# Kernel optimization log

Measured on AMD Instinct MI355X. Metric: run time of the kernel, lower is better.

The kernel has to match this reference:

```python
import jax, jax.numpy as jnp
import numpy as np

NL = 256
NP = 8192
NV = 16
B = 2


def _xavier(key, shape):
    fan_in, fan_out = shape[-2], shape[-1]
    lim = np.sqrt(6.0 / (fan_in + fan_out))
    return jax.random.uniform(key, shape, jnp.float32, -lim, lim)


def setup_inputs() -> dict:
    key = jax.random.key(0)
    ks = jax.random.split(key, 12)
    return {
        "nodes": jax.random.normal(ks[0], (B, NP, NL), jnp.float32),
        "edges_attributes": jax.random.normal(ks[1], (NP, NV, NL), jnp.float32),
        "edges_indices": jax.random.randint(ks[2], (NP, NV), 0, NP, jnp.int64) if jax.config.jax_enable_x64 else jax.random.randint(ks[2], (NP, NV), 0, NP).astype(jnp.int32),
        # edge MLP (dim_in=3*NL, nb_hidden=3 -> first + 2 hidden + last)
        "e_fw": _xavier(ks[3], (3 * NL, NL)), "e_fb": jnp.zeros((NL,), jnp.float32),
        "e_hw": _xavier(ks[4], (2, NL, NL)), "e_hb": jnp.zeros((2, NL), jnp.float32),
        "e_lw": _xavier(ks[5], (NL, NL)), "e_lb": jnp.zeros((NL,), jnp.float32),
        # node MLP (dim_in=2*NL)
        "n_fw": _xavier(ks[6], (2 * NL, NL)), "n_fb": jnp.zeros((NL,), jnp.float32),
        "n_hw": _xavier(ks[7], (2, NL, NL)), "n_hb": jnp.zeros((2, NL), jnp.float32),
        "n_lw": _xavier(ks[8], (NL, NL)), "n_lb": jnp.zeros((NL,), jnp.float32),
    }


def _mlp(x, fw, fb, hw, hb, lw, lb):
    x = jax.nn.relu(x @ fw + fb)
    for i in range(hw.shape[0]):  # fixed small number of hidden layers
        x = jax.nn.relu(x @ hw[i] + hb[i])
    return x @ lw + lb


def reference(nodes, edges_attributes, edges_indices,
              e_fw, e_fb, e_hw, e_hb, e_lw, e_lb,
              n_fw, n_fb, n_hw, n_hb, n_lw, n_lb):
    b, npts, nl = nodes.shape
    nv = edges_indices.shape[1]
    # gather neighbor features: [B, Np, Nv, Nl]
    nodes_nb = jnp.take(nodes, edges_indices, axis=1)
    # self features broadcast over neighbor axis, edge attrs broadcast over batch
    self_exp = jnp.broadcast_to(nodes[:, :, None, :], (b, npts, nv, nl))
    edge_exp = jnp.broadcast_to(edges_attributes[None], (b, npts, nv, nl))
    concat_msg = jnp.concatenate([self_exp, nodes_nb, edge_exp], axis=-1)  # [B,Np,Nv,3Nl]
    new_edges = _mlp(concat_msg, e_fw, e_fb, e_hw, e_hb, e_lw, e_lb)  # [B,Np,Nv,Nl]
    agg = jnp.sum(new_edges, axis=2)  # [B,Np,Nl]
    concat_nodes = jnp.concatenate([nodes, agg], axis=-1)  # [B,Np,2Nl]
    new_nodes = nodes + _mlp(concat_nodes, n_fw, n_fb, n_hw, n_hb, n_lw, n_lb)
    return new_nodes, new_edges[0]
```

## Files before the change

### kernel.cpp

```cpp
#include <hip/hip_runtime.h>
#include <hip/hip_bf16.h>


typedef __bf16 bf16;
typedef __bf16 bf16x8 __attribute__((ext_vector_type(8)));
typedef float f32x4 __attribute__((ext_vector_type(4)));

#define MFMA16(a, b, c) __builtin_amdgcn_mfma_f32_16x16x32_bf16((a), (b), (c), 0, 0, 0)

constexpr int kNP = 8192;
constexpr int kNV = 16;

__global__ __launch_bounds__(256) void pack_all(
    const float* __restrict__ e_fw, const float* __restrict__ e_hw,
    const float* __restrict__ e_lw, const float* __restrict__ n_fw,
    const float* __restrict__ n_hw, const float* __restrict__ n_lw,
    bf16* __restrict__ wp) {
  int t = blockIdx.x * 256 + threadIdx.x;
  const float* src;
  int kd = 8, local;
  if (t < 196608) {
    src = e_fw + (t >> 16) * 65536; local = t & 65535;
  } else if (t < 262144) { src = e_hw;           local = t - 196608;
  } else if (t < 327680) { src = e_hw + 65536;   local = t - 262144;
  } else if (t < 393216) { src = e_lw;           local = t - 327680;
  } else if (t < 524288) { src = n_fw;           local = t - 393216; kd = 16;
  } else if (t < 589824) { src = n_hw;           local = t - 524288;
  } else if (t < 655360) { src = n_hw + 65536;   local = t - 589824;
  } else               { src = n_lw;             local = t - 655360; }
  int j = local & 7;
  int l = (local >> 3) & 63;
  int r2 = local >> 9;
  int ks = r2 % kd;
  int nt = r2 / kd;
  int k = ks * 32 + ((l >> 4) << 3) + j;
  int n = (nt << 4) + (l & 15);
  wp[t] = (bf16)src[k * 256 + n];
}

template <int KD, int MT>
__device__ __forceinline__ void layer_acc(const bf16* X, int xs,
                                          const bf16* __restrict__ Wp,
                                          const float* __restrict__ bias,
                                          f32x4 (&acc)[MT][4], int rowOff,
                                          int wc) {
  const int lane = threadIdx.x & 63;
  const int q = lane >> 4;
  const int c = lane & 15;
#pragma unroll
  for (int nt = 0; nt < 4; nt++) {
    float bv = bias ? bias[wc * 64 + nt * 16 + c] : 0.0f;
#pragma unroll
    for (int mt = 0; mt < MT; mt++) {
      acc[mt][nt][0] = bv; acc[mt][nt][1] = bv;
      acc[mt][nt][2] = bv; acc[mt][nt][3] = bv;
    }
  }
#pragma unroll
  for (int ks = 0; ks < KD; ks++) {
    bf16x8 a[MT];
#pragma unroll
    for (int mt = 0; mt < MT; mt++)
      a[mt] = *(const bf16x8*)(X + (rowOff + mt * 16 + c) * xs + ks * 32 + q * 8);
    bf16x8 bb[4];
#pragma unroll
    for (int nt = 0; nt < 4; nt++)
      bb[nt] = *(const bf16x8*)(Wp + ((((wc * 4 + nt) * KD + ks) * 64 + lane) << 3));
#pragma unroll
    for (int mt = 0; mt < MT; mt++)
#pragma unroll
      for (int nt = 0; nt < 4; nt++)
        acc[mt][nt] = MFMA16(a[mt], bb[nt], acc[mt][nt]);
  }
}

template <int KD, int MT, bool RELU>
__device__ __forceinline__ void layer_inplace(bf16* X, int xs_r, int xs_w,
                                              const bf16* __restrict__ Wp,
                                              const float* __restrict__ bias,
                                              int rowOff, int wc) {
  f32x4 acc[MT][4];
  layer_acc<KD, MT>(X, xs_r, Wp, bias, acc, rowOff, wc);
  const int lane = threadIdx.x & 63;
  const int q = lane >> 4;
  const int c = lane & 15;
  __syncthreads();
#pragma unroll
  for (int mt = 0; mt < MT; mt++)
#pragma unroll
    for (int nt = 0; nt < 4; nt++)
#pragma unroll
      for (int i = 0; i < 4; i++) {
        float v = acc[mt][nt][i];
        if (RELU) v = fmaxf(v, 0.0f);
        X[(rowOff + mt * 16 + q * 4 + i) * xs_w + (wc * 64 + nt * 16 + c)] = (bf16)v;
      }
  __syncthreads();
}

__global__ __launch_bounds__(512, 4) void producer_sp(
    const float* __restrict__ nodes, const bf16* __restrict__ w_self,
    const bf16* __restrict__ w_nb, const float* __restrict__ e_fb,
    bf16* __restrict__ Sb, bf16* __restrict__ Pb) {
  __shared__ bf16 X[64 * 280];
  const int t = threadIdx.x;
  const int m0 = blockIdx.x * 64;
  {
    const int r = t >> 3;
    const int q8 = t & 7;
#pragma unroll
    for (int c8 = 0; c8 < 4; c8++) {
      int col = q8 * 8 + c8 * 64;
      float4 f0 = *(const float4*)(nodes + (m0 + r) * 256 + col);
      float4 f1 = *(const float4*)(nodes + (m0 + r) * 256 + col + 4);
      bf16x8 v;
      v[0] = (bf16)f0.x; v[1] = (bf16)f0.y; v[2] = (bf16)f0.z; v[3] = (bf16)f0.w;
      v[4] = (bf16)f1.x; v[5] = (bf16)f1.y; v[6] = (bf16)f1.z; v[7] = (bf16)f1.w;
      *(bf16x8*)(X + r * 280 + col) = v;
    }
  }
  __syncthreads();
  const int lane = t & 63;
  const int w = t >> 6;
  const int wc = w & 3;
  const int rowOff = (w >> 2) * 32;
  const int q = lane >> 4;
  const int c = lane & 15;
  f32x4 acc[2][4];
  layer_acc<8, 2>(X, 280, w_self, e_fb, acc, rowOff, wc);
#pragma unroll
  for (int mt = 0; mt < 2; mt++)
#pragma unroll
    for (int nt = 0; nt < 4; nt++)
#pragma unroll
      for (int i = 0; i < 4; i++)
        Sb[(m0 + rowOff + mt * 16 + q * 4 + i) * 256 + wc * 64 + nt * 16 + c] =
            (bf16)acc[mt][nt][i];
  layer_acc<8, 2>(X, 280, w_nb, nullptr, acc, rowOff, wc);
#pragma unroll
  for (int mt = 0; mt < 2; mt++)
#pragma unroll
    for (int nt = 0; nt < 4; nt++)
#pragma unroll
      for (int i = 0; i < 4; i++)
        Pb[(m0 + rowOff + mt * 16 + q * 4 + i) * 256 + wc * 64 + nt * 16 + c] =
            (bf16)acc[mt][nt][i];
}

__global__ __launch_bounds__(512, 4) void edge_mlp(
    const bf16* __restrict__ S, const bf16* __restrict__ P,
    const float* __restrict__ eattr, const int* __restrict__ idx,
    const bf16* __restrict__ w_ea, const bf16* __restrict__ Wh0,
    const bf16* __restrict__ Wh1, const bf16* __restrict__ Wl,
    const float* __restrict__ e_hb, const float* __restrict__ e_lb,
    bf16* __restrict__ agg, float* __restrict__ out_edges) {
  __shared__ bf16 X[64 * 280];
  const int t = threadIdx.x;
  const int pbase = blockIdx.x * 2;
  {
    const int r = t >> 4;
    const int q16 = t & 15;
    const float* src = eattr + (pbase * 16 + r) * 256 + q16 * 16;
    bf16* dst = X + (32 + r) * 280 + q16 * 16;
    float4 f0 = *(const float4*)(src);
    float4 f1 = *(const float4*)(src + 4);
    float4 f2 = *(const float4*)(src + 8);
    float4 f3 = *(const float4*)(src + 12);
    bf16x8 v0, v1;
    v0[0] = (bf16)f0.x; v0[1] = (bf16)f0.y; v0[2] = (bf16)f0.z; v0[3] = (bf16)f0.w;
    v0[4] = (bf16)f1.x; v0[5] = (bf16)f1.y; v0[6] = (bf16)f1.z; v0[7] = (bf16)f1.w;
    v1[0] = (bf16)f2.x; v1[1] = (bf16)f2.y; v1[2] = (bf16)f2.z; v1[3] = (bf16)f2.w;
    v1[4] = (bf16)f3.x; v1[5] = (bf16)f3.y; v1[6] = (bf16)f3.z; v1[7] = (bf16)f3.w;
    *(bf16x8*)(dst) = v0;
    *(bf16x8*)(dst + 8) = v1;
  }
  __syncthreads();
  const int lane = t & 63;
  const int w = t >> 6;
  const int wc = w & 3;
  const int rg = w >> 2;
  const int q = lane >> 4;
  const int c = lane & 15;
  {
    f32x4 acce[1][4];
    layer_acc<8, 1>(X, 280, w_ea, nullptr, acce, 32 + rg * 16, wc);
    __syncthreads();
#pragma unroll
    for (int nt = 0; nt < 4; nt++)
#pragma unroll
      for (int i = 0; i < 4; i++)
        X[(32 + rg * 16 + q * 4 + i) * 280 + wc * 64 + nt * 16 + c] =
            (bf16)acce[0][nt][i];
  }
  __syncthreads();
  {
    const int r = t >> 3;
    const int q8 = t & 7;
    const int b = r >> 5;
    const int rr = r & 31;
    const int p = pbase + (rr >> 4);
    const int v = rr & 15;
    const int nb = idx[p * kNV + v];
    const bf16* Srow = S + ((b << 13) + p) * 256;
    const bf16* Prow = P + ((b << 13) + nb) * 256;
    bf16x8 hold[4];
#pragma unroll
    for (int j = 0; j < 4; j++) {
      int col = q8 * 32 + j * 8;
      bf16x8 ev = *(const bf16x8*)(X + (32 + rr) * 280 + col);
      bf16x8 sv = *(const bf16x8*)(Srow + col);
      bf16x8 pv = *(const bf16x8*)(Prow + col);
      bf16x8 o;
#pragma unroll
      for (int k = 0; k < 8; k++) {
        float f = (float)sv[k] + (float)pv[k] + (float)ev[k];
        o[k] = (bf16)fmaxf(f, 0.0f);
      }
      hold[j] = o;
    }
    __syncthreads();
#pragma unroll
    for (int j = 0; j < 4; j++)
      *(bf16x8*)(X + r * 280 + q8 * 32 + j * 8) = hold[j];
  }
  __syncthreads();
  layer_inplace<8, 2, true>(X, 280, 280, Wh0, e_hb, rg * 32, wc);
  layer_inplace<8, 2, true>(X, 280, 280, Wh1, e_hb + 256, rg * 32, wc);
  f32x4 acc[2][4];
  layer_acc<8, 2>(X, 280, Wl, e_lb, acc, rg * 32, wc);
#pragma unroll
  for (int mt = 0; mt < 2; mt++) {
    const int g = rg * 2 + mt;
#pragma unroll
    for (int nt = 0; nt < 4; nt++) {
      float s = acc[mt][nt][0] + acc[mt][nt][1] + acc[mt][nt][2] + acc[mt][nt][3];
      s += __shfl_xor(s, 16, 64);
      s += __shfl_xor(s, 32, 64);
      if (lane < 16)
        agg[(((g >> 1) << 13) + pbase + (g & 1)) * 256 + wc * 64 + nt * 16 + lane] =
            (bf16)s;
    }
  }
  if (rg == 0) {
#pragma unroll
    for (int mt = 0; mt < 2; mt++)
#pragma unroll
      for (int nt = 0; nt < 4; nt++)
#pragma unroll
        for (int i = 0; i < 4; i++) {
          int e = (pbase + mt) * kNV + q * 4 + i;
          out_edges[e * 256 + wc * 64 + nt * 16 + c] = acc[mt][nt][i];
        }
  }
}

__global__ __launch_bounds__(512, 4) void node_mlp(
    const float* __restrict__ nodes, const bf16* __restrict__ agg,
    const bf16* __restrict__ Wf, const bf16* __restrict__ Wh0,
    const bf16* __restrict__ Wh1, const bf16* __restrict__ Wl,
    const float* __restrict__ n_fb, const float* __restrict__ n_hb,
    const float* __restrict__ n_lb, float* __restrict__ out_nodes) {
  __shared__ bf16 X[32 * 536];
  const int t = threadIdx.x;
  const int r = t >> 4;
  const int q16 = t & 15;
  const int m = blockIdx.x * 32 + r;
#pragma unroll
  for (int c8 = 0; c8 < 4; c8++) {
    int col = q16 * 8 + c8 * 128;
    if (col < 256) {
      float4 f0 = *(const float4*)(nodes + m * 256 + col);
      float4 f1 = *(const float4*)(nodes + m * 256 + col + 4);
      bf16x8 v;
      v[0] = (bf16)f0.x; v[1] = (bf16)f0.y; v[2] = (bf16)f0.z; v[3] = (bf16)f0.w;
      v[4] = (bf16)f1.x; v[5] = (bf16)f1.y; v[6] = (bf16)f1.z; v[7] = (bf16)f1.w;
      *(bf16x8*)(X + r * 536 + col) = v;
    } else {
      *(bf16x8*)(X + r * 536 + col) =
          *(const bf16x8*)(agg + m * 256 + (col - 256));
    }
  }
  __syncthreads();
  const int w = t >> 6;
  const int wc = w & 3;
  const int rowOff = (w >> 2) * 16;
  layer_inplace<16, 1, true>(X, 536, 280, Wf, n_fb, rowOff, wc);
  layer_inplace<8, 1, true>(X, 280, 280, Wh0, n_hb, rowOff, wc);
  layer_inplace<8, 1, true>(X, 280, 280, Wh1, n_hb + 256, rowOff, wc);
  f32x4 acc[1][4];
  layer_acc<8, 1>(X, 280, Wl, n_lb, acc, rowOff, wc);
  const int lane = t & 63;
  const int q = lane >> 4;
  const int c = lane & 15;
#pragma unroll
  for (int nt = 0; nt < 4; nt++)
#pragma unroll
    for (int i = 0; i < 4; i++) {
      int mm = blockIdx.x * 32 + rowOff + q * 4 + i;
      int col = wc * 64 + nt * 16 + c;
      out_nodes[mm * 256 + col] = nodes[mm * 256 + col] + acc[0][nt][i];
    }
}

extern "C" void kernel_launch(void* const* d_in, const int* in_sizes, int n_in,
                              void* d_out, int out_size, void* d_ws,
                              size_t ws_size, hipStream_t stream) {
  const float* nodes = (const float*)d_in[0];
  const float* eattr = (const float*)d_in[1];
  const int* eidx = (const int*)d_in[2];
  const float* e_fw = (const float*)d_in[3];
  const float* e_fb = (const float*)d_in[4];
  const float* e_hw = (const float*)d_in[5];
  const float* e_hb = (const float*)d_in[6];
  const float* e_lw = (const float*)d_in[7];
  const float* e_lb = (const float*)d_in[8];
  const float* n_fw = (const float*)d_in[9];
  const float* n_fb = (const float*)d_in[10];
  const float* n_hw = (const float*)d_in[11];
  const float* n_hb = (const float*)d_in[12];
  const float* n_lw = (const float*)d_in[13];
  const float* n_lb = (const float*)d_in[14];

  char* ws = (char*)d_ws;
  bf16* Sb = (bf16*)(ws + 0);
  bf16* Pb = (bf16*)(ws + 8388608);
  bf16* aggb = (bf16*)(ws + 16777216);
  bf16* wp = (bf16*)(ws + 25165824);
  bf16* w_self = wp;
  bf16* w_nb = wp + 65536;
  bf16* w_ea = wp + 131072;
  bf16* w_eh0 = wp + 196608;
  bf16* w_eh1 = wp + 262144;
  bf16* w_el = wp + 327680;
  bf16* w_nf = wp + 393216;
  bf16* w_nh0 = wp + 524288;
  bf16* w_nh1 = wp + 589824;
  bf16* w_nl = wp + 655360;

  float* out_nodes = (float*)d_out;
  float* out_edges = (float*)d_out + 4194304;

  pack_all<<<2816, 256, 0, stream>>>(e_fw, e_hw, e_lw, n_fw, n_hw, n_lw, wp);
  producer_sp<<<256, 512, 0, stream>>>(nodes, w_self, w_nb, e_fb, Sb, Pb);
  edge_mlp<<<4096, 512, 0, stream>>>(Sb, Pb, eattr, eidx, w_ea, w_eh0, w_eh1,
                                     w_el, e_hb, e_lb, aggb, out_edges);
  node_mlp<<<512, 512, 0, stream>>>(nodes, aggb, w_nf, w_nh0, w_nh1, w_nl,
                                    n_fb, n_hb, n_lb, out_nodes);
}
```

Baseline: 470.9 us.

## Halve block sizes across kernels and vectorize weight packing per MFMA tile

```diff
diff --git a/kernel.cpp b/kernel.cpp
--- a/kernel.cpp
+++ b/kernel.cpp
@@ -16,26 +16,32 @@
     const float* __restrict__ e_lw, const float* __restrict__ n_fw,
     const float* __restrict__ n_hw, const float* __restrict__ n_lw,
     bf16* __restrict__ wp) {
-  int t = blockIdx.x * 256 + threadIdx.x;
+  const int s = blockIdx.x;
   const float* src;
-  int kd = 8, local;
-  if (t < 196608) {
-    src = e_fw + (t >> 16) * 65536; local = t & 65535;
-  } else if (t < 262144) { src = e_hw;           local = t - 196608;
-  } else if (t < 327680) { src = e_hw + 65536;   local = t - 262144;
-  } else if (t < 393216) { src = e_lw;           local = t - 327680;
-  } else if (t < 524288) { src = n_fw;           local = t - 393216; kd = 16;
-  } else if (t < 589824) { src = n_hw;           local = t - 524288;
-  } else if (t < 655360) { src = n_hw + 65536;   local = t - 589824;
-  } else               { src = n_lw;             local = t - 655360; }
-  int j = local & 7;
-  int l = (local >> 3) & 63;
-  int r2 = local >> 9;
-  int ks = r2 % kd;
-  int nt = r2 / kd;
-  int k = ks * 32 + ((l >> 4) << 3) + j;
-  int n = (nt << 4) + (l & 15);
-  wp[t] = (bf16)src[k * 256 + n];
+  bf16* dst;
+  int ks, kd = 8;
+  if (s < 24)      { src = e_fw + (s >> 3) * 65536; dst = wp + (s >> 3) * 65536; ks = s & 7; }
+  else if (s < 32) { src = e_hw;          dst = wp + 196608; ks = s - 24; }
+  else if (s < 40) { src = e_hw + 65536;  dst = wp + 262144; ks = s - 32; }
+  else if (s < 48) { src = e_lw;          dst = wp + 327680; ks = s - 40; }
+  else if (s < 64) { src = n_fw;          dst = wp + 393216; ks = s - 48; kd = 16; }
+  else if (s < 72) { src = n_hw;          dst = wp + 524288; ks = s - 64; }
+  else if (s < 80) { src = n_hw + 65536;  dst = wp + 589824; ks = s - 72; }
+  else             { src = n_lw;          dst = wp + 655360; ks = s - 80; }
+  const int t = threadIdx.x;
+  const int lane = t & 63;
+  const int w = t >> 6;
+  const int q = lane >> 4;
+  const int c = lane & 15;
+#pragma unroll
+  for (int nti = 0; nti < 4; nti++) {
+    const int nt = w * 4 + nti;
+    bf16x8 v;
+#pragma unroll
+    for (int j = 0; j < 8; j++)
+      v[j] = (bf16)src[(ks * 32 + q * 8 + j) * 256 + nt * 16 + c];
+    *(bf16x8*)(dst + (((nt * kd + ks) * 64 + lane) << 3)) = v;
+  }
 }
 
 template <int KD, int MT>
@@ -98,70 +104,18 @@
   __syncthreads();
 }
 
-__global__ __launch_bounds__(512, 4) void producer_sp(
+__global__ __launch_bounds__(256, 8) void producer_sp(
     const float* __restrict__ nodes, const bf16* __restrict__ w_self,
     const bf16* __restrict__ w_nb, const float* __restrict__ e_fb,
     bf16* __restrict__ Sb, bf16* __restrict__ Pb) {
-  __shared__ bf16 X[64 * 280];
+  __shared__ bf16 X[16 * 280];
   const int t = threadIdx.x;
-  const int m0 = blockIdx.x * 64;
-  {
-    const int r = t >> 3;
-    const int q8 = t & 7;
-#pragma unroll
-    for (int c8 = 0; c8 < 4; c8++) {
-      int col = q8 * 8 + c8 * 64;
-      float4 f0 = *(const float4*)(nodes + (m0 + r) * 256 + col);
-      float4 f1 = *(const float4*)(nodes + (m0 + r) * 256 + col + 4);
-      bf16x8 v;
-      v[0] = (bf16)f0.x; v[1] = (bf16)f0.y; v[2] = (bf16)f0.z; v[3] = (bf16)f0.w;
-      v[4] = (bf16)f1.x; v[5] = (bf16)f1.y; v[6] = (bf16)f1.z; v[7] = (bf16)f1.w;
-      *(bf16x8*)(X + r * 280 + col) = v;
-    }
-  }
-  __syncthreads();
-  const int lane = t & 63;
-  const int w = t >> 6;
-  const int wc = w & 3;
-  const int rowOff = (w >> 2) * 32;
-  const int q = lane >> 4;
-  const int c = lane & 15;
-  f32x4 acc[2][4];
-  layer_acc<8, 2>(X, 280, w_self, e_fb, acc, rowOff, wc);
-#pragma unroll
-  for (int mt = 0; mt < 2; mt++)
-#pragma unroll
-    for (int nt = 0; nt < 4; nt++)
-#pragma unroll
-      for (int i = 0; i < 4; i++)
-        Sb[(m0 + rowOff + mt * 16 + q * 4 + i) * 256 + wc * 64 + nt * 16 + c] =
-            (bf16)acc[mt][nt][i];
-  layer_acc<8, 2>(X, 280, w_nb, nullptr, acc, rowOff, wc);
-#pragma unroll
-  for (int mt = 0; mt < 2; mt++)
-#pragma unroll
-    for (int nt = 0; nt < 4; nt++)
-#pragma unroll
-      for (int i = 0; i < 4; i++)
-        Pb[(m0 + rowOff + mt * 16 + q * 4 + i) * 256 + wc * 64 + nt * 16 + c] =
-            (bf16)acc[mt][nt][i];
-}
-
-__global__ __launch_bounds__(512, 4) void edge_mlp(
-    const bf16* __restrict__ S, const bf16* __restrict__ P,
-    const float* __restrict__ eattr, const int* __restrict__ idx,
-    const bf16* __restrict__ w_ea, const bf16* __restrict__ Wh0,
-    const bf16* __restrict__ Wh1, const bf16* __restrict__ Wl,
-    const float* __restrict__ e_hb, const float* __restrict__ e_lb,
-    bf16* __restrict__ agg, float* __restrict__ out_edges) {
-  __shared__ bf16 X[64 * 280];
-  const int t = threadIdx.x;
-  const int pbase = blockIdx.x * 2;
+  const int m0 = blockIdx.x * 16;
   {
     const int r = t >> 4;
     const int q16 = t & 15;
-    const float* src = eattr + (pbase * 16 + r) * 256 + q16 * 16;
-    bf16* dst = X + (32 + r) * 280 + q16 * 16;
+    const float* src = nodes + (m0 + r) * 256 + q16 * 16;
+    bf16* dst = X + r * 280 + q16 * 16;
     float4 f0 = *(const float4*)(src);
     float4 f1 = *(const float4*)(src + 4);
     float4 f2 = *(const float4*)(src + 8);
@@ -176,30 +130,72 @@
   }
   __syncthreads();
   const int lane = t & 63;
-  const int w = t >> 6;
-  const int wc = w & 3;
-  const int rg = w >> 2;
+  const int wc = t >> 6;
+  const int q = lane >> 4;
+  const int c = lane & 15;
+  f32x4 acc[1][4];
+  layer_acc<8, 1>(X, 280, w_self, e_fb, acc, 0, wc);
+#pragma unroll
+  for (int nt = 0; nt < 4; nt++)
+#pragma unroll
+    for (int i = 0; i < 4; i++)
+      Sb[(m0 + q * 4 + i) * 256 + wc * 64 + nt * 16 + c] = (bf16)acc[0][nt][i];
+  layer_acc<8, 1>(X, 280, w_nb, nullptr, acc, 0, wc);
+#pragma unroll
+  for (int nt = 0; nt < 4; nt++)
+#pragma unroll
+    for (int i = 0; i < 4; i++)
+      Pb[(m0 + q * 4 + i) * 256 + wc * 64 + nt * 16 + c] = (bf16)acc[0][nt][i];
+}
+
+__global__ __launch_bounds__(256, 6) void edge_mlp(
+    const bf16* __restrict__ S, const bf16* __restrict__ P,
+    const float* __restrict__ eattr, const int* __restrict__ idx,
+    const bf16* __restrict__ w_ea, const bf16* __restrict__ Wh0,
+    const bf16* __restrict__ Wh1, const bf16* __restrict__ Wl,
+    const float* __restrict__ e_hb, const float* __restrict__ e_lb,
+    bf16* __restrict__ agg, float* __restrict__ out_edges) {
+  __shared__ bf16 X[32 * 280];
+  const int t = threadIdx.x;
+  const int p = blockIdx.x;
+  {
+    const int r = t >> 4;
+    const int q16 = t & 15;
+    const float* src = eattr + (p * 16 + r) * 256 + q16 * 16;
+    bf16* dst = X + (16 + r) * 280 + q16 * 16;
+    float4 f0 = *(const float4*)(src);
+    float4 f1 = *(const float4*)(src + 4);
+    float4 f2 = *(const float4*)(src + 8);
+    float4 f3 = *(const float4*)(src + 12);
+    bf16x8 v0, v1;
+    v0[0] = (bf16)f0.x; v0[1] = (bf16)f0.y; v0[2] = (bf16)f0.z; v0[3] = (bf16)f0.w;
+    v0[4] = (bf16)f1.x; v0[5] = (bf16)f1.y; v0[6] = (bf16)f1.z; v0[7] = (bf16)f1.w;
+    v1[0] = (bf16)f2.x; v1[1] = (bf16)f2.y; v1[2] = (bf16)f2.z; v1[3] = (bf16)f2.w;
+    v1[4] = (bf16)f3.x; v1[5] = (bf16)f3.y; v1[6] = (bf16)f3.z; v1[7] = (bf16)f3.w;
+    *(bf16x8*)(dst) = v0;
+    *(bf16x8*)(dst + 8) = v1;
+  }
+  __syncthreads();
+  const int lane = t & 63;
+  const int wc = t >> 6;
   const int q = lane >> 4;
   const int c = lane & 15;
   {
     f32x4 acce[1][4];
-    layer_acc<8, 1>(X, 280, w_ea, nullptr, acce, 32 + rg * 16, wc);
+    layer_acc<8, 1>(X, 280, w_ea, nullptr, acce, 16, wc);
     __syncthreads();
 #pragma unroll
     for (int nt = 0; nt < 4; nt++)
 #pragma unroll
       for (int i = 0; i < 4; i++)
-        X[(32 + rg * 16 + q * 4 + i) * 280 + wc * 64 + nt * 16 + c] =
-            (bf16)acce[0][nt][i];
+        X[(16 + q * 4 + i) * 280 + wc * 64 + nt * 16 + c] = (bf16)acce[0][nt][i];
   }
   __syncthreads();
   {
     const int r = t >> 3;
     const int q8 = t & 7;
-    const int b = r >> 5;
-    const int rr = r & 31;
-    const int p = pbase + (rr >> 4);
-    const int v = rr & 15;
+    const int b = r >> 4;
+    const int v = r & 15;
     const int nb = idx[p * kNV + v];
     const bf16* Srow = S + ((b << 13) + p) * 256;
     const bf16* Prow = P + ((b << 13) + nb) * 256;
@@ -207,7 +203,7 @@
 #pragma unroll
     for (int j = 0; j < 4; j++) {
       int col = q8 * 32 + j * 8;
-      bf16x8 ev = *(const bf16x8*)(X + (32 + rr) * 280 + col);
+      bf16x8 ev = *(const bf16x8*)(X + (16 + v) * 280 + col);
       bf16x8 sv = *(const bf16x8*)(Srow + col);
       bf16x8 pv = *(const bf16x8*)(Prow + col);
       bf16x8 o;
@@ -224,71 +220,67 @@
       *(bf16x8*)(X + r * 280 + q8 * 32 + j * 8) = hold[j];
   }
   __syncthreads();
-  layer_inplace<8, 2, true>(X, 280, 280, Wh0, e_hb, rg * 32, wc);
-  layer_inplace<8, 2, true>(X, 280, 280, Wh1, e_hb + 256, rg * 32, wc);
+  layer_inplace<8, 2, true>(X, 280, 280, Wh0, e_hb, 0, wc);
+  layer_inplace<8, 2, true>(X, 280, 280, Wh1, e_hb + 256, 0, wc);
   f32x4 acc[2][4];
-  layer_acc<8, 2>(X, 280, Wl, e_lb, acc, rg * 32, wc);
+  layer_acc<8, 2>(X, 280, Wl, e_lb, acc, 0, wc);
 #pragma unroll
   for (int mt = 0; mt < 2; mt++) {
-    const int g = rg * 2 + mt;
 #pragma unroll
     for (int nt = 0; nt < 4; nt++) {
       float s = acc[mt][nt][0] + acc[mt][nt][1] + acc[mt][nt][2] + acc[mt][nt][3];
       s += __shfl_xor(s, 16, 64);
       s += __shfl_xor(s, 32, 64);
       if (lane < 16)
-        agg[(((g >> 1) << 13) + pbase + (g & 1)) * 256 + wc * 64 + nt * 16 + lane] =
-            (bf16)s;
-    }
-  }
-  if (rg == 0) {
-#pragma unroll
-    for (int mt = 0; mt < 2; mt++)
-#pragma unroll
-      for (int nt = 0; nt < 4; nt++)
-#pragma unroll
-        for (int i = 0; i < 4; i++) {
-          int e = (pbase + mt) * kNV + q * 4 + i;
-          out_edges[e * 256 + wc * 64 + nt * 16 + c] = acc[mt][nt][i];
-        }
-  }
-}
-
-__global__ __launch_bounds__(512, 4) void node_mlp(
+        agg[((mt << 13) + p) * 256 + wc * 64 + nt * 16 + lane] = (bf16)s;
+    }
+  }
+#pragma unroll
+  for (int nt = 0; nt < 4; nt++)
+#pragma unroll
+    for (int i = 0; i < 4; i++) {
+      int e = p * kNV + q * 4 + i;
+      out_edges[e * 256 + wc * 64 + nt * 16 + c] = acc[0][nt][i];
+    }
+}
+
+__global__ __launch_bounds__(256, 8) void node_mlp(
     const float* __restrict__ nodes, const bf16* __restrict__ agg,
     const bf16* __restrict__ Wf, const bf16* __restrict__ Wh0,
     const bf16* __restrict__ Wh1, const bf16* __restrict__ Wl,
     const float* __restrict__ n_fb, const float* __restrict__ n_hb,
     const float* __restrict__ n_lb, float* __restrict__ out_nodes) {
-  __shared__ bf16 X[32 * 536];
+  __shared__ bf16 X[16 * 536];
   const int t = threadIdx.x;
   const int r = t >> 4;
   const int q16 = t & 15;
-  const int m = blockIdx.x * 32 + r;
-#pragma unroll
-  for (int c8 = 0; c8 < 4; c8++) {
-    int col = q16 * 8 + c8 * 128;
-    if (col < 256) {
-      float4 f0 = *(const float4*)(nodes + m * 256 + col);
-      float4 f1 = *(const float4*)(nodes + m * 256 + col + 4);
+  const int m = blockIdx.x * 16 + r;
+  if (q16 < 8) {
+    const float* src = nodes + m * 256 + q16 * 32;
+    bf16* dst = X + r * 536 + q16 * 32;
+#pragma unroll
+    for (int h = 0; h < 4; h++) {
+      float4 f0 = *(const float4*)(src + h * 8);
+      float4 f1 = *(const float4*)(src + h * 8 + 4);
       bf16x8 v;
       v[0] = (bf16)f0.x; v[1] = (bf16)f0.y; v[2] = (bf16)f0.z; v[3] = (bf16)f0.w;
       v[4] = (bf16)f1.x; v[5] = (bf16)f1.y; v[6] = (bf16)f1.z; v[7] = (bf16)f1.w;
-      *(bf16x8*)(X + r * 536 + col) = v;
-    } else {
-      *(bf16x8*)(X + r * 536 + col) =
-          *(const bf16x8*)(agg + m * 256 + (col - 256));
-    }
-  }
-  __syncthreads();
-  const int w = t >> 6;
-  const int wc = w & 3;
-  const int rowOff = (w >> 2) * 16;
-  layer_inplace<16, 1, true>(X, 536, 280, Wf, n_fb, rowOff, wc);
-  layer_inplace<8, 1, true>(X, 280, 280, Wh0, n_hb, rowOff, wc);
-  layer_inplace<8, 1, true>(X, 280, 280, Wh1, n_hb + 256, rowOff, wc);
+      *(bf16x8*)(dst + h * 8) = v;
+    }
+  } else {
+    const bf16* src = agg + m * 256 + (q16 - 8) * 32;
+    bf16* dst = X + r * 536 + 256 + (q16 - 8) * 32;
+#pragma unroll
+    for (int h = 0; h < 4; h++)
+      *(bf16x8*)(dst + h * 8) = *(const bf16x8*)(src + h * 8);
+  }
+  __syncthreads();
+  const int wc = t >> 6;
+  layer_inplace<16, 1, true>(X, 536, 280, Wf, n_fb, 0, wc);
+  layer_inplace<8, 1, true>(X, 280, 280, Wh0, n_hb, 0, wc);
+  layer_inplace<8, 1, true>(X, 280, 280, Wh1, n_hb + 256, 0, wc);
   f32x4 acc[1][4];
-  layer_acc<8, 1>(X, 280, Wl, n_lb, acc, rowOff, wc);
+  layer_acc<8, 1>(X, 280, Wl, n_lb, acc, 0, wc);
   const int lane = t & 63;
   const int q = lane >> 4;
   const int c = lane & 15;
@@ -296,7 +288,7 @@
   for (int nt = 0; nt < 4; nt++)
 #pragma unroll
     for (int i = 0; i < 4; i++) {
-      int mm = blockIdx.x * 32 + rowOff + q * 4 + i;
+      int mm = blockIdx.x * 16 + q * 4 + i;
       int col = wc * 64 + nt * 16 + c;
       out_nodes[mm * 256 + col] = nodes[mm * 256 + col] + acc[0][nt][i];
     }
@@ -340,10 +332,10 @@
   float* out_nodes = (float*)d_out;
   float* out_edges = (float*)d_out + 4194304;
 
-  pack_all<<<2816, 256, 0, stream>>>(e_fw, e_hw, e_lw, n_fw, n_hw, n_lw, wp);
-  producer_sp<<<256, 512, 0, stream>>>(nodes, w_self, w_nb, e_fb, Sb, Pb);
-  edge_mlp<<<4096, 512, 0, stream>>>(Sb, Pb, eattr, eidx, w_ea, w_eh0, w_eh1,
+  pack_all<<<88, 256, 0, stream>>>(e_fw, e_hw, e_lw, n_fw, n_hw, n_lw, wp);
+  producer_sp<<<1024, 256, 0, stream>>>(nodes, w_self, w_nb, e_fb, Sb, Pb);
+  edge_mlp<<<8192, 256, 0, stream>>>(Sb, Pb, eattr, eidx, w_ea, w_eh0, w_eh1,
                                      w_el, e_hb, e_lb, aggb, out_edges);
-  node_mlp<<<512, 512, 0, stream>>>(nodes, aggb, w_nf, w_nh0, w_nh1, w_nl,
-                                    n_fb, n_hb, n_lb, out_nodes);
-}
+  node_mlp<<<1024, 256, 0, stream>>>(nodes, aggb, w_nf, w_nh0, w_nh1, w_nl,
+                                     n_fb, n_hb, n_lb, out_nodes);
+}
```

Result: slower. 556.4 us (+18.1%).

## Use 32x32x16 MFMA for edge MLP hidden and last layers with repacked weights

Applied to the files above, without the earlier changes.

```diff
diff --git a/kernel.cpp b/kernel.cpp
--- a/kernel.cpp
+++ b/kernel.cpp
@@ -5,8 +5,10 @@
 typedef __bf16 bf16;
 typedef __bf16 bf16x8 __attribute__((ext_vector_type(8)));
 typedef float f32x4 __attribute__((ext_vector_type(4)));
+typedef float f32x16 __attribute__((ext_vector_type(16)));
 
 #define MFMA16(a, b, c) __builtin_amdgcn_mfma_f32_16x16x32_bf16((a), (b), (c), 0, 0, 0)
+#define MFMA32(a, b, c) __builtin_amdgcn_mfma_f32_32x32x16_bf16((a), (b), (c), 0, 0, 0)
 
 constexpr int kNP = 8192;
 constexpr int kNV = 16;
@@ -16,26 +18,49 @@
     const float* __restrict__ e_lw, const float* __restrict__ n_fw,
     const float* __restrict__ n_hw, const float* __restrict__ n_lw,
     bf16* __restrict__ wp) {
-  int t = blockIdx.x * 256 + threadIdx.x;
-  const float* src;
-  int kd = 8, local;
-  if (t < 196608) {
-    src = e_fw + (t >> 16) * 65536; local = t & 65535;
-  } else if (t < 262144) { src = e_hw;           local = t - 196608;
-  } else if (t < 327680) { src = e_hw + 65536;   local = t - 262144;
-  } else if (t < 393216) { src = e_lw;           local = t - 327680;
-  } else if (t < 524288) { src = n_fw;           local = t - 393216; kd = 16;
-  } else if (t < 589824) { src = n_hw;           local = t - 524288;
-  } else if (t < 655360) { src = n_hw + 65536;   local = t - 589824;
-  } else               { src = n_lw;             local = t - 655360; }
-  int j = local & 7;
-  int l = (local >> 3) & 63;
-  int r2 = local >> 9;
-  int ks = r2 % kd;
-  int nt = r2 / kd;
-  int k = ks * 32 + ((l >> 4) << 3) + j;
-  int n = (nt << 4) + (l & 15);
-  wp[t] = (bf16)src[k * 256 + n];
+  const int s = blockIdx.x;
+  const int t = threadIdx.x;
+  const int lane = t & 63;
+  const int w = t >> 6;
+  if (s < 64) {
+    const float* src;
+    bf16* dst;
+    int ks, kd = 8;
+    if (s < 24)      { src = e_fw + (s >> 3) * 65536; dst = wp + (s >> 3) * 65536; ks = s & 7; }
+    else if (s < 40) { src = n_fw;          dst = wp + 393216; ks = s - 24; kd = 16; }
+    else if (s < 48) { src = n_hw;          dst = wp + 524288; ks = s - 40; }
+    else if (s < 56) { src = n_hw + 65536;  dst = wp + 589824; ks = s - 48; }
+    else             { src = n_lw;          dst = wp + 655360; ks = s - 56; }
+    const int q = lane >> 4;
+    const int c = lane & 15;
+#pragma unroll
+    for (int nti = 0; nti < 4; nti++) {
+      const int nt = w * 4 + nti;
+      bf16x8 v;
+#pragma unroll
+      for (int j = 0; j < 8; j++)
+        v[j] = (bf16)src[(ks * 32 + q * 8 + j) * 256 + nt * 16 + c];
+      *(bf16x8*)(dst + (((nt * kd + ks) * 64 + lane) << 3)) = v;
+    }
+  } else {
+    const int s2 = s - 64;
+    const int mat = s2 >> 4;
+    const int ks = s2 & 15;
+    const float* src = (mat == 0) ? e_hw : (mat == 1) ? (e_hw + 65536) : e_lw;
+    bf16* dst = wp + 196608 + mat * 65536;
+    const int ko = lane >> 5;
+    const int col = lane & 31;
+#pragma unroll
+    for (int h = 0; h < 2; h++) {
+      const int wcnt = w * 2 + h;
+      bf16x8 v;
+#pragma unroll
+      for (int j = 0; j < 8; j++)
+        v[j] = (bf16)src[(ks * 16 + ko * 8 + j) * 256 + wcnt * 32 + col];
+      *(bf16x8*)(dst + (((wcnt * 16 + ks) * 64 + lane) << 3));
+      *(bf16x8*)(dst + (((wcnt * 16 + ks) * 64 + lane) << 3)) = v;
+    }
+  }
 }
 
 template <int KD, int MT>
@@ -95,6 +120,56 @@
         if (RELU) v = fmaxf(v, 0.0f);
         X[(rowOff + mt * 16 + q * 4 + i) * xs_w + (wc * 64 + nt * 16 + c)] = (bf16)v;
       }
+  __syncthreads();
+}
+
+template <int KD2>
+__device__ __forceinline__ void layer_acc32(const bf16* X, int xs,
+                                            const bf16* __restrict__ Wp,
+                                            const float* __restrict__ bias,
+                                            f32x16 (&acc)[2], int rowOff,
+                                            int wc) {
+  const int lane = threadIdx.x & 63;
+  const int row = lane & 31;
+  const int ko = lane >> 5;
+  const int col = lane & 31;
+#pragma unroll
+  for (int nt = 0; nt < 2; nt++) {
+    float bv = bias ? bias[wc * 64 + nt * 32 + col] : 0.0f;
+#pragma unroll
+    for (int r = 0; r < 16; r++) acc[nt][r] = bv;
+  }
+#pragma unroll
+  for (int ks = 0; ks < KD2; ks++) {
+    bf16x8 a = *(const bf16x8*)(X + (rowOff + row) * xs + ks * 16 + ko * 8);
+#pragma unroll
+    for (int nt = 0; nt < 2; nt++) {
+      bf16x8 b = *(const bf16x8*)(Wp + ((((wc * 2 + nt) * KD2 + ks) * 64 + lane) << 3));
+      acc[nt] = MFMA32(a, b, acc[nt]);
+    }
+  }
+}
+
+template <int KD2, bool RELU>
+__device__ __forceinline__ void layer_inplace32(bf16* X, int xs,
+                                                const bf16* __restrict__ Wp,
+                                                const float* __restrict__ bias,
+                                                int rowOff, int wc) {
+  f32x16 acc[2];
+  layer_acc32<KD2>(X, xs, Wp, bias, acc, rowOff, wc);
+  const int lane = threadIdx.x & 63;
+  const int h = lane >> 5;
+  const int col = lane & 31;
+  __syncthreads();
+#pragma unroll
+  for (int nt = 0; nt < 2; nt++)
+#pragma unroll
+    for (int r = 0; r < 16; r++) {
+      float v = acc[nt][r];
+      if (RELU) v = fmaxf(v, 0.0f);
+      const int rr = (r & 3) + 8 * (r >> 2) + 4 * h;
+      X[(rowOff + rr) * xs + (wc * 64 + nt * 32 + col)] = (bf16)v;
+    }
   __syncthreads();
 }
 
@@ -224,33 +299,32 @@
       *(bf16x8*)(X + r * 280 + q8 * 32 + j * 8) = hold[j];
   }
   __syncthreads();
-  layer_inplace<8, 2, true>(X, 280, 280, Wh0, e_hb, rg * 32, wc);
-  layer_inplace<8, 2, true>(X, 280, 280, Wh1, e_hb + 256, rg * 32, wc);
-  f32x4 acc[2][4];
-  layer_acc<8, 2>(X, 280, Wl, e_lb, acc, rg * 32, wc);
-#pragma unroll
-  for (int mt = 0; mt < 2; mt++) {
-    const int g = rg * 2 + mt;
-#pragma unroll
-    for (int nt = 0; nt < 4; nt++) {
-      float s = acc[mt][nt][0] + acc[mt][nt][1] + acc[mt][nt][2] + acc[mt][nt][3];
-      s += __shfl_xor(s, 16, 64);
+  layer_inplace32<16, true>(X, 280, Wh0, e_hb, rg * 32, wc);
+  layer_inplace32<16, true>(X, 280, Wh1, e_hb + 256, rg * 32, wc);
+  f32x16 acc[2];
+  layer_acc32<16>(X, 280, Wl, e_lb, acc, rg * 32, wc);
+  const int col = lane & 31;
+#pragma unroll
+  for (int nt = 0; nt < 2; nt++) {
+#pragma unroll
+    for (int pp = 0; pp < 2; pp++) {
+      float s = 0.0f;
+#pragma unroll
+      for (int r8 = 0; r8 < 8; r8++) s += acc[nt][pp * 8 + r8];
       s += __shfl_xor(s, 32, 64);
-      if (lane < 16)
-        agg[(((g >> 1) << 13) + pbase + (g & 1)) * 256 + wc * 64 + nt * 16 + lane] =
-            (bf16)s;
+      if (lane < 32)
+        agg[((rg << 13) + pbase + pp) * 256 + wc * 64 + nt * 32 + col] = (bf16)s;
     }
   }
   if (rg == 0) {
-#pragma unroll
-    for (int mt = 0; mt < 2; mt++)
-#pragma unroll
-      for (int nt = 0; nt < 4; nt++)
-#pragma unroll
-        for (int i = 0; i < 4; i++) {
-          int e = (pbase + mt) * kNV + q * 4 + i;
-          out_edges[e * 256 + wc * 64 + nt * 16 + c] = acc[mt][nt][i];
-        }
+    const int h = lane >> 5;
+#pragma unroll
+    for (int nt = 0; nt < 2; nt++)
+#pragma unroll
+      for (int r = 0; r < 16; r++) {
+        const int rr = (r & 3) + 8 * (r >> 2) + 4 * h;
+        out_edges[(pbase * 16 + rr) * 256 + wc * 64 + nt * 32 + col] = acc[nt][r];
+      }
   }
 }
 
@@ -340,7 +414,7 @@
   float* out_nodes = (float*)d_out;
   float* out_edges = (float*)d_out + 4194304;
 
-  pack_all<<<2816, 256, 0, stream>>>(e_fw, e_hw, e_lw, n_fw, n_hw, n_lw, wp);
+  pack_all<<<112, 256, 0, stream>>>(e_fw, e_hw, e_lw, n_fw, n_hw, n_lw, wp);
   producer_sp<<<256, 512, 0, stream>>>(nodes, w_self, w_nb, e_fb, Sb, Pb);
   edge_mlp<<<4096, 512, 0, stream>>>(Sb, Pb, eattr, eidx, w_ea, w_eh0, w_eh1,
                                      w_el, e_hb, e_lb, aggb, out_edges);
```

New measurement: 470.8 us. About the same (-0.0%).
